# Performance work log

Hardware: AMD Instinct MI355X
Metric: run time of the kernel (lower is better)

The kernel has to match this reference:

```python
import jax, jax.numpy as jnp
import numpy as np

N = 50000      # nodes
E = 800000     # edges
GENE = 64      # gene_dim
HID = 128      # hidden_dim
NCLS = 10      # num_classes
EPS = 1e-5


def setup_inputs() -> dict:
    key = jax.random.key(0)
    ks = jax.random.split(key, 4)
    inp = {
        "x": jax.random.normal(ks[0], (N, GENE), jnp.float32),
        "edge_index": jax.random.randint(ks[1], (2, E), 0, N),
    }
    # PNA-style conv: concat([x, 4 aggregators x 3 scalers]) -> 13*d_in features
    dims = [(GENE, HID), (HID, 2 * HID), (2 * HID, HID), (HID, HID // 2)]
    for i, (din, dout) in enumerate(dims, 1):
        k = jax.random.fold_in(key, i)
        inp[f"W{i}"] = jax.random.normal(k, (13 * din, dout), jnp.float32) / float(np.sqrt(13 * din))
        inp[f"b{i}"] = jnp.zeros((dout,), jnp.float32)
        inp[f"gamma{i}"] = jnp.ones((dout,), jnp.float32)
        inp[f"beta{i}"] = jnp.zeros((dout,), jnp.float32)
    inp["Wc"] = jax.random.normal(ks[2], (HID // 2, NCLS), jnp.float32) / float(np.sqrt(HID // 2))
    inp["bc"] = jnp.zeros((NCLS,), jnp.float32)
    return inp


def _pna(x, src, dst, deg, log_deg, delta, W, b):
    # gather source features along edges: [E, d]
    msg = x[src]
    cnt = jnp.maximum(deg, 1.0)[:, None]
    s = jax.ops.segment_sum(msg, dst, num_segments=N)
    mean = s / cnt
    mean_sq = jax.ops.segment_sum(msg * msg, dst, num_segments=N) / cnt
    std = jnp.sqrt(jnp.maximum(mean_sq - mean * mean, 0.0) + EPS)
    has = (deg > 0)[:, None]
    mn = jnp.where(has, jax.ops.segment_min(msg, dst, num_segments=N), 0.0)
    mx = jnp.where(has, jax.ops.segment_max(msg, dst, num_segments=N), 0.0)
    aggs = jnp.concatenate([mean, mn, mx, std], axis=-1)  # [N, 4d]
    amp = (log_deg / delta)[:, None]                       # amplification scaler
    att = jnp.where(log_deg > 0, delta / jnp.maximum(log_deg, 1e-6), 1.0)[:, None]
    feat = jnp.concatenate([x, aggs, aggs * amp, aggs * att], axis=-1)  # [N, 13d]
    return feat @ W + b


def _bn(h, gamma, beta):
    m = h.mean(axis=0)
    v = h.var(axis=0)
    return (h - m) / jnp.sqrt(v + EPS) * gamma + beta


def reference(x, edge_index, W1, b1, gamma1, beta1, W2, b2, gamma2, beta2,
              W3, b3, gamma3, beta3, W4, b4, gamma4, beta4, Wc, bc):
    src, dst = edge_index[0], edge_index[1]
    deg = jax.ops.segment_sum(jnp.ones((E,), jnp.float32), dst, num_segments=N)
    log_deg = jnp.log1p(deg)
    delta = log_deg.mean()
    h = _pna(x, src, dst, deg, log_deg, delta, W1, b1)
    h = _bn(jax.nn.relu(h), gamma1, beta1)
    h = _pna(h, src, dst, deg, log_deg, delta, W2, b2)
    h = _bn(jax.nn.relu(h), gamma2, beta2)
    h = _pna(h, src, dst, deg, log_deg, delta, W3, b3)
    h = _bn(jax.nn.relu(h), gamma3, beta3)
    h = _pna(h, src, dst, deg, log_deg, delta, W4, b4)
    h = _bn(jax.nn.relu(h), gamma4, beta4)
    return h @ Wc + bc
```

## Files before the change

kernel.cpp:

```cpp
#include <hip/hip_runtime.h>
#include <hip/hip_bf16.h>

#define NN 50000
#define NE 800000
#define EPSV 1e-5f
#define NB 49

typedef _Float16 h8 __attribute__((ext_vector_type(8)));
typedef float    f4 __attribute__((ext_vector_type(4)));


__global__ void k_deg(const int* __restrict__ dst, int* __restrict__ deg){
  int e = blockIdx.x*blockDim.x + threadIdx.x;
  if(e < NE) atomicAdd(&deg[dst[e]], 1);
}

__global__ void k_logdeg(const int* __restrict__ deg, float* __restrict__ logdeg,
                         float* __restrict__ dsum){
  int i = blockIdx.x*blockDim.x + threadIdx.x;
  float v = 0.f;
  if(i < NN){ v = log1pf((float)deg[i]); logdeg[i] = v; }
  __shared__ float sh[256];
  sh[threadIdx.x] = v; __syncthreads();
  for(int off=128; off>0; off>>=1){
    if(threadIdx.x < off) sh[threadIdx.x] += sh[threadIdx.x+off];
    __syncthreads();
  }
  if(threadIdx.x == 0) atomicAdd(dsum, sh[0]);
}

__global__ void k_scalers(const float* __restrict__ logdeg, const float* __restrict__ dsum,
                          float* __restrict__ amp, float* __restrict__ att){
  int i = blockIdx.x*blockDim.x + threadIdx.x;
  if(i >= NN) return;
  float delta = dsum[0] / (float)NN;
  float ld = logdeg[i];
  amp[i] = ld / delta;
  att[i] = (ld > 0.f) ? (delta / fmaxf(ld, 1e-6f)) : 1.f;
}

__global__ void k_scan1(const int* __restrict__ deg, int* __restrict__ rowptr,
                        int* __restrict__ bsum){
  __shared__ int buf[1024];
  int tid = threadIdx.x;
  int i = blockIdx.x*1024 + tid;
  int v = (i < NN) ? deg[i] : 0;
  buf[tid] = v; __syncthreads();
  for(int off=1; off<1024; off<<=1){
    int t = (tid >= off) ? buf[tid-off] : 0;
    __syncthreads();
    buf[tid] += t;
    __syncthreads();
  }
  if(i < NN) rowptr[i] = buf[tid] - v;
  if(tid == 1023) bsum[blockIdx.x] = buf[1023];
}

__global__ void k_scan2(int* __restrict__ bsum){
  if(threadIdx.x == 0){
    int s = 0;
    for(int b = 0; b < NB; b++){ int t = bsum[b]; bsum[b] = s; s += t; }
    bsum[NB] = s;
  }
}

__global__ void k_scan3(int* __restrict__ rowptr, int* __restrict__ cursor,
                        const int* __restrict__ bsum){
  int i = blockIdx.x*256 + threadIdx.x;
  if(i < NN){
    int v = rowptr[i] + bsum[i >> 10];
    rowptr[i] = v; cursor[i] = v;
  }
  if(i == NN) rowptr[NN] = bsum[NB];
}

__global__ void k_fill(const int* __restrict__ src, const int* __restrict__ dst,
                       int* __restrict__ cursor, int* __restrict__ colidx){
  int e = blockIdx.x*blockDim.x + threadIdx.x;
  if(e < NE){
    int pos = atomicAdd(&cursor[dst[e]], 1);
    colidx[pos] = src[e];
  }
}

__global__ void k_cvtx(const float* __restrict__ x, _Float16* __restrict__ act){
  int i = blockIdx.x*256 + threadIdx.x;
  if(i < NN*64) act[i] = (_Float16)x[i];
}

__global__ void k_coef_id(float* __restrict__ cs, float* __restrict__ csh,
                          _Float16* __restrict__ cs16, _Float16* __restrict__ csh16){
  int c = threadIdx.x;
  cs[c] = 1.f; csh[c] = 0.f;
  cs16[c] = (_Float16)1.f; csh16[c] = (_Float16)0.f;
}

__global__ void k_bn_coef(const float* __restrict__ colsum, const float* __restrict__ colss,
                          const float* __restrict__ gamma, const float* __restrict__ beta,
                          int dout, float* __restrict__ cs, float* __restrict__ csh,
                          _Float16* __restrict__ cs16, _Float16* __restrict__ csh16){
  int c = threadIdx.x;
  if(c >= dout) return;
  float mean = colsum[c] / (float)NN;
  float var  = colss[c] / (float)NN - mean*mean;
  float inv  = rsqrtf(fmaxf(var, 0.f) + EPSV);
  float a = inv * gamma[c];
  float b = beta[c] - mean * a;
  cs[c] = a; csh[c] = b;
  cs16[c] = (_Float16)a; csh16[c] = (_Float16)b;
}


template<int D>
__global__ __launch_bounds__(256) void k_agg8(
    const _Float16* __restrict__ act,
    const int* __restrict__ rowptr, const int* __restrict__ colidx,
    const float* __restrict__ cs, const float* __restrict__ csh,
    _Float16* __restrict__ aggs, size_t aggN)
{
  constexpr int LPN = D >> 3;
  constexpr int NPW = 64 / LPN;
  int wv = threadIdx.x >> 6, lane = threadIdx.x & 63;
  int n = blockIdx.x*(NPW*4) + wv*NPW + (lane / LPN);
  int c = (lane % LPN) * 8;
  if(n >= NN) return;
  int beg = rowptr[n], end = rowptr[n+1];
  const _Float16* hp = act + c;

  float s[8], q[8], mn[8], mx[8];
  #pragma unroll
  for(int j = 0; j < 8; j++){ s[j]=0.f; q[j]=0.f; mn[j]=INFINITY; mx[j]=-INFINITY; }

#define ACC8(v) { _Pragma("unroll") for(int j=0;j<8;j++){ float a=(float)(v)[j]; \
    s[j]+=a; q[j]+=a*a; mn[j]=fminf(mn[j],a); mx[j]=fmaxf(mx[j],a); } }

  int e = beg;
  for(; e+8 <= end; e+=8){
    int i0=colidx[e],   i1=colidx[e+1], i2=colidx[e+2], i3=colidx[e+3];
    int i4=colidx[e+4], i5=colidx[e+5], i6=colidx[e+6], i7=colidx[e+7];
    h8 v0 = *(const h8*)(hp + (size_t)i0*D);
    h8 v1 = *(const h8*)(hp + (size_t)i1*D);
    h8 v2 = *(const h8*)(hp + (size_t)i2*D);
    h8 v3 = *(const h8*)(hp + (size_t)i3*D);
    h8 v4 = *(const h8*)(hp + (size_t)i4*D);
    h8 v5 = *(const h8*)(hp + (size_t)i5*D);
    h8 v6 = *(const h8*)(hp + (size_t)i6*D);
    h8 v7 = *(const h8*)(hp + (size_t)i7*D);
    ACC8(v0) ACC8(v1) ACC8(v2) ACC8(v3) ACC8(v4) ACC8(v5) ACC8(v6) ACC8(v7)
  }
  for(; e+4 <= end; e+=4){
    int i0=colidx[e], i1=colidx[e+1], i2=colidx[e+2], i3=colidx[e+3];
    h8 v0 = *(const h8*)(hp + (size_t)i0*D);
    h8 v1 = *(const h8*)(hp + (size_t)i1*D);
    h8 v2 = *(const h8*)(hp + (size_t)i2*D);
    h8 v3 = *(const h8*)(hp + (size_t)i3*D);
    ACC8(v0) ACC8(v1) ACC8(v2) ACC8(v3)
  }
  for(; e < end; e++){
    h8 v = *(const h8*)(hp + (size_t)colidx[e]*D);
    ACC8(v)
  }
#undef ACC8

  float cnt = (end>beg) ? (float)(end-beg) : 1.f;
  h8 vm, vn, vx, vs;
  #pragma unroll
  for(int j = 0; j < 8; j++){
    float a = cs[c+j], b = csh[c+j];
    float mean_r = s[j]/cnt;
    float var_r  = fmaxf(q[j]/cnt - mean_r*mean_r, 0.f);
    float meanp = a*mean_r + b;
    float mnp = (a >= 0.f) ? a*mn[j]+b : a*mx[j]+b;
    float mxp = (a >= 0.f) ? a*mx[j]+b : a*mn[j]+b;
    float sdp = sqrtf(a*a*var_r + EPSV);
    if(end <= beg){ meanp = 0.f; mnp = 0.f; mxp = 0.f; sdp = sqrtf(EPSV); }
    vm[j] = (_Float16)meanp; vn[j] = (_Float16)mnp;
    vx[j] = (_Float16)mxp;   vs[j] = (_Float16)sdp;
  }

  _Float16* dst = aggs + (size_t)(c>>6)*aggN + (size_t)n*256 + (c & 63);
  *(h8*)(dst)       = vm;
  *(h8*)(dst + 64)  = vn;
  *(h8*)(dst + 128) = vx;
  *(h8*)(dst + 192) = vs;
}


struct PackJob { const float* W; _Float16* dst; int d, o, j0, start; };
struct PackArgs { PackJob job[9]; int total; };

__global__ void k_pack_all(PackArgs a){
  int idx = blockIdx.x*256 + threadIdx.x;
  if(idx >= a.total) return;
  int ji = 0;
  while(ji < 8 && idx >= a.job[ji+1].start) ji++;
  PackJob J = a.job[ji];
  int rel = idx - J.start;
  int j    = rel & 7;
  int lane = (rel >> 3) & 63;
  int rem  = rel >> 9;
  int ntiles = J.o >> 4;
  int kb = rem / ntiles;
  int nt = rem - kb*ntiles;
  int k = kb*32 + (lane>>4)*8 + j;
  int n = nt*16 + (lane&15);
  int srcrow;
  if(k < 64)       srcrow = J.j0 + k;
  else if(k < 320){ int t=k-64;  srcrow = (1+(t>>6))*J.d + J.j0 + (t&63); }
  else if(k < 576){ int t=k-320; srcrow = (5+(t>>6))*J.d + J.j0 + (t&63); }
  else            { int t=k-576; srcrow = (9+(t>>6))*J.d + J.j0 + (t&63); }
  J.dst[rel] = (_Float16)J.W[(size_t)srcrow*J.o + n];
}


template<int NCH>
__global__ __launch_bounds__(256) void k_mfma_fused(
    const _Float16* __restrict__ actIn,
    const _Float16* __restrict__ aggs,
    const float* __restrict__ amp, const float* __restrict__ att,
    const _Float16* __restrict__ cs16, const _Float16* __restrict__ csh16,
    const _Float16* __restrict__ Wp, int o,
    const float* __restrict__ bias,
    _Float16* __restrict__ out,
    float* __restrict__ colsum, float* __restrict__ colss)
{
  constexpr int D = NCH * 64;
  __shared__ float redS[64], redQ[64];
  int tid  = threadIdx.x;
  int wv   = tid >> 6;
  int lane = tid & 63;
  int mi   = lane & 15;
  int q    = lane >> 4;
  int m0   = blockIdx.y * 128 + wv * 32;
  int c0   = blockIdx.x * 64;
  int ntiles = o >> 4;
  int nt0  = blockIdx.x * 4;

  if(tid < 64){ redS[tid] = 0.f; redQ[tid] = 0.f; }

  int mrow[2];
  mrow[0] = min(m0 + mi,      NN-1);
  mrow[1] = min(m0 + 16 + mi, NN-1);
  _Float16 am16[2] = { (_Float16)amp[mrow[0]], (_Float16)amp[mrow[1]] };
  _Float16 at16[2] = { (_Float16)att[mrow[0]], (_Float16)att[mrow[1]] };
  const _Float16* hAb[2];
  const _Float16* agb[2];
  hAb[0] = actIn + (size_t)mrow[0]*D + q*8;
  hAb[1] = actIn + (size_t)mrow[1]*D + q*8;
  agb[0] = aggs + (size_t)mrow[0]*256 + q*8;
  agb[1] = aggs + (size_t)mrow[1]*256 + q*8;

  f4 acc[2][4] = {};
  const size_t aggN = (size_t)NN*256;

  #pragma unroll
  for(int c = 0; c < NCH; c++){
    const _Float16* Wpc = Wp + (size_t)c*832*o;
    auto bfrag = [&](int kb, int nn) -> h8 {
      return *(const h8*)(Wpc + (((size_t)kb*ntiles + nt0 + nn)*64 + lane)*8);
    };

    h8 ax[2][2];
    h8 ag[8][2];
    #pragma unroll
    for(int kb = 0; kb < 2; kb++){
      h8 sc = *(const h8*)(cs16  + c*64 + kb*32 + q*8);
      h8 sh = *(const h8*)(csh16 + c*64 + kb*32 + q*8);
      #pragma unroll
      for(int t = 0; t < 2; t++){
        h8 a = *(const h8*)(hAb[t] + c*64 + kb*32);
        ax[kb][t] = a*sc + sh;
      }
    }
    #pragma unroll
    for(int idx = 0; idx < 8; idx++)
      #pragma unroll
      for(int t = 0; t < 2; t++)
        ag[idx][t] = *(const h8*)(agb[t] + (size_t)c*aggN + idx*32);

    #pragma unroll
    for(int kb = 0; kb < 2; kb++)
      #pragma unroll
      for(int t = 0; t < 2; t++)
        #pragma unroll
        for(int nn = 0; nn < 4; nn++)
          acc[t][nn] = __builtin_amdgcn_mfma_f32_16x16x32_f16(ax[kb][t], bfrag(kb,nn), acc[t][nn], 0,0,0);

    #pragma unroll
    for(int idx = 0; idx < 8; idx++){
      #pragma unroll
      for(int t = 0; t < 2; t++){
        h8 apl = ag[idx][t];
        h8 aam = apl * am16[t];
        h8 aat = apl * at16[t];
        #pragma unroll
        for(int nn = 0; nn < 4; nn++){
          acc[t][nn] = __builtin_amdgcn_mfma_f32_16x16x32_f16(apl, bfrag(2+idx,  nn), acc[t][nn], 0,0,0);
          acc[t][nn] = __builtin_amdgcn_mfma_f32_16x16x32_f16(aam, bfrag(10+idx, nn), acc[t][nn], 0,0,0);
          acc[t][nn] = __builtin_amdgcn_mfma_f32_16x16x32_f16(aat, bfrag(18+idx, nn), acc[t][nn], 0,0,0);
        }
      }
    }
  }

  __syncthreads();

  #pragma unroll
  for(int nn = 0; nn < 4; nn++){
    int n = c0 + nn*16 + mi;
    float bv = bias[n];
    float ps = 0.f, pq = 0.f;
    #pragma unroll
    for(int t = 0; t < 2; t++){
      #pragma unroll
      for(int r = 0; r < 4; r++){
        int m = m0 + t*16 + q*4 + r;
        if(m < NN){
          float v = fmaxf(bv + acc[t][nn][r], 0.f);
          out[(size_t)m*o + n] = (_Float16)v;
          ps += v; pq += v*v;
        }
      }
    }
    ps += __shfl_xor(ps, 16); pq += __shfl_xor(pq, 16);
    ps += __shfl_xor(ps, 32); pq += __shfl_xor(pq, 32);
    if(q == 0){
      atomicAdd(&redS[nn*16 + mi], ps);
      atomicAdd(&redQ[nn*16 + mi], pq);
    }
  }
  __syncthreads();
  if(tid < 64){
    atomicAdd(&colsum[c0 + tid], redS[tid]);
    atomicAdd(&colss[c0 + tid],  redQ[tid]);
  }
}


__global__ __launch_bounds__(256) void k_cls(const _Float16* __restrict__ h,
    const float* __restrict__ cs, const float* __restrict__ csh,
    const float* __restrict__ Wc, const float* __restrict__ bc,
    float* __restrict__ out){
  __shared__ float w[640];
  __shared__ float bb[16];
  __shared__ float sca[64], shb[64];
  int tid = threadIdx.x;
  for(int i = tid; i < 640; i += 256) w[i] = Wc[i];
  if(tid < 10) bb[tid] = bc[tid];
  if(tid < 64){ sca[tid] = cs[tid]; shb[tid] = csh[tid]; }
  __syncthreads();
  int idx = blockIdx.x*256 + tid;
  int n = idx >> 4;
  int c = idx & 15;
  if(n < NN && c < 10){
    float acc = bb[c];
    const _Float16* hp = h + (size_t)n*64;
    #pragma unroll
    for(int k = 0; k < 64; k++)
      acc += ((float)hp[k]*sca[k] + shb[k]) * w[k*10 + c];
    out[(size_t)n*10 + c] = acc;
  }
}


extern "C" void kernel_launch(void* const* d_in, const int* in_sizes, int n_in,
                              void* d_out, int out_size, void* d_ws, size_t ws_size,
                              hipStream_t stream){
  const float* x = (const float*)d_in[0];
  const int* edge = (const int*)d_in[1];
  const int* esrc = edge;
  const int* edst = edge + NE;
  const float* W[4]  = {(const float*)d_in[2],  (const float*)d_in[6],
                        (const float*)d_in[10], (const float*)d_in[14]};
  const float* bb[4] = {(const float*)d_in[3],  (const float*)d_in[7],
                        (const float*)d_in[11], (const float*)d_in[15]};
  const float* gm[4] = {(const float*)d_in[4],  (const float*)d_in[8],
                        (const float*)d_in[12], (const float*)d_in[16]};
  const float* bt[4] = {(const float*)d_in[5],  (const float*)d_in[9],
                        (const float*)d_in[13], (const float*)d_in[17]};
  const float* Wc = (const float*)d_in[18];
  const float* bc = (const float*)d_in[19];
  (void)in_sizes; (void)n_in; (void)out_size; (void)ws_size;

  char* p = (char*)d_ws;
  auto alloc = [&](size_t bytes)->char*{
    char* r = p; p += (bytes + 255) & ~(size_t)255; return r;
  };
  _Float16* act0 = (_Float16*)alloc((size_t)NN*256*2);
  _Float16* act1 = (_Float16*)alloc((size_t)NN*256*2);
  _Float16* aggs = (_Float16*)alloc((size_t)4*NN*256*2);
  int*   deg    = (int*)  alloc((size_t)NN*4);
  float* logdeg = (float*)alloc((size_t)NN*4);
  float* amp    = (float*)alloc((size_t)NN*4);
  float* att    = (float*)alloc((size_t)NN*4);
  int*   rowptr = (int*)  alloc((size_t)(NN+1)*4);
  int*   cursor = (int*)  alloc((size_t)NN*4);
  int*   colidx = (int*)  alloc((size_t)NE*4);
  int*   bsum   = (int*)  alloc((size_t)(NB+1)*4);
  float* colsumL= (float*)alloc(4*256*4);
  float* colssL = (float*)alloc(4*256*4);
  float* dsum   = (float*)alloc(256);
  float*    csA  = (float*)   alloc(256*4);
  float*    cshA = (float*)   alloc(256*4);
  float*    csB  = (float*)   alloc(256*4);
  float*    cshB = (float*)   alloc(256*4);
  _Float16* cs16A  = (_Float16*)alloc(256*2);
  _Float16* csh16A = (_Float16*)alloc(256*2);
  _Float16* cs16B  = (_Float16*)alloc(256*2);
  _Float16* csh16B = (_Float16*)alloc(256*2);

  const int din[4]  = {64, 128, 256, 128};
  const int dto[4]  = {128, 256, 128, 64};
  const size_t aggN = (size_t)NN*256;
  _Float16* WpL[4];
  PackArgs pa; int pj = 0, poff = 0;
  for(int l = 0; l < 4; l++){
    int nch = din[l]/64;
    WpL[l] = (_Float16*)alloc((size_t)nch*832*dto[l]*2);
    for(int c = 0; c < nch; c++){
      pa.job[pj] = { W[l], WpL[l] + (size_t)c*832*dto[l], din[l], dto[l], c*64, poff };
      poff += 832*dto[l]; pj++;
    }
  }
  pa.total = poff;

  hipMemsetAsync(deg, 0, (size_t)NN*4, stream);
  hipMemsetAsync(dsum, 0, 4, stream);
  hipMemsetAsync(colsumL, 0, 4*256*4, stream);
  hipMemsetAsync(colssL,  0, 4*256*4, stream);

  k_pack_all<<<(pa.total+255)/256, 256, 0, stream>>>(pa);
  k_deg     <<<(NE+255)/256, 256, 0, stream>>>(edst, deg);
  k_logdeg  <<<(NN+255)/256, 256, 0, stream>>>(deg, logdeg, dsum);
  k_scalers <<<(NN+255)/256, 256, 0, stream>>>(logdeg, dsum, amp, att);
  k_scan1   <<<NB, 1024, 0, stream>>>(deg, rowptr, bsum);
  k_scan2   <<<1, 64, 0, stream>>>(bsum);
  k_scan3   <<<(NN+256)/256, 256, 0, stream>>>(rowptr, cursor, bsum);
  k_fill    <<<(NE+255)/256, 256, 0, stream>>>(esrc, edst, cursor, colidx);
  k_cvtx    <<<(NN*64+255)/256, 256, 0, stream>>>(x, act0);
  k_coef_id <<<1, 256, 0, stream>>>(csA, cshA, cs16A, csh16A);

  _Float16* actIn = act0;  _Float16* actOut = act1;
  float *csI = csA, *cshI = cshA, *csO = csB, *cshO = cshB;
  _Float16 *cs16I = cs16A, *csh16I = csh16A, *cs16O = cs16B, *csh16O = csh16B;

  for(int l = 0; l < 4; l++){
    int d = din[l], o = dto[l];
    int npb = (64 / (d >> 3)) * 4;
    int nagg = (NN + npb - 1) / npb;
    dim3 g(o/64, (NN+127)/128);
    float* csum = colsumL + l*256;
    float* csq  = colssL + l*256;
    switch(d){
      case 64:
        k_agg8<64><<<nagg, 256, 0, stream>>>(actIn, rowptr, colidx, csI, cshI, aggs, aggN);
        k_mfma_fused<1><<<g, 256, 0, stream>>>(actIn, aggs, amp, att, cs16I, csh16I,
                                               WpL[l], o, bb[l], actOut, csum, csq);
        break;
      case 128:
        k_agg8<128><<<nagg, 256, 0, stream>>>(actIn, rowptr, colidx, csI, cshI, aggs, aggN);
        k_mfma_fused<2><<<g, 256, 0, stream>>>(actIn, aggs, amp, att, cs16I, csh16I,
                                               WpL[l], o, bb[l], actOut, csum, csq);
        break;
      default:
        k_agg8<256><<<nagg, 256, 0, stream>>>(actIn, rowptr, colidx, csI, cshI, aggs, aggN);
        k_mfma_fused<4><<<g, 256, 0, stream>>>(actIn, aggs, amp, att, cs16I, csh16I,
                                               WpL[l], o, bb[l], actOut, csum, csq);
        break;
    }
    k_bn_coef<<<1, 256, 0, stream>>>(csum, csq, gm[l], bt[l], o,
                                     csO, cshO, cs16O, csh16O);
    _Float16* ta = actIn; actIn = actOut; actOut = ta;
    float* tf;
    tf = csI;  csI = csO;  csO = tf;
    tf = cshI; cshI = cshO; cshO = tf;
    _Float16* th;
    th = cs16I;  cs16I = cs16O;  cs16O = th;
    th = csh16I; csh16I = csh16O; csh16O = th;
  }
  k_cls<<<(NN*16+255)/256, 256, 0, stream>>>(actIn, csI, cshI, Wc, bc, (float*)d_out);
}
```

Baseline: 698.4 us.

## Double-buffer MFMA weight fragments in LDS via async global_load_lds

The fused PNA matmul kernel now stages weight B-fragments into a double-buffered shared-memory tile using asynchronous global-to-LDS loads, one phase ahead. The A operands (activations and aggregates) are also prefetched into registers for the next phase. The K loop is restructured into 9 phases per 64-wide chunk, with a block barrier after each phase. The aim is to overlap weight and activation loads with MFMA work and share weights across the four waves. The cost is many more barriers, extra LDS traffic, and lower register-level prefetch depth than the old approach of loading all aggregates at once.

Result: faster. 656.0 us (-6.1%).

```diff
diff --git a/kernel.cpp b/kernel.cpp
--- a/kernel.cpp
+++ b/kernel.cpp
@@ -8,6 +8,13 @@
 
 typedef _Float16 h8 __attribute__((ext_vector_type(8)));
 typedef float    f4 __attribute__((ext_vector_type(4)));
+
+#define AS1 __attribute__((address_space(1)))
+#define AS3 __attribute__((address_space(3)))
+
+__device__ __forceinline__ void gload_lds16(const _Float16* g, _Float16* l){
+  __builtin_amdgcn_global_load_lds((const AS1 void*)g, (AS3 void*)l, 16, 0, 0);
+}
 
 
 __global__ void k_deg(const int* __restrict__ dst, int* __restrict__ deg){
@@ -222,9 +229,12 @@
     const _Float16* __restrict__ Wp, int o,
     const float* __restrict__ bias,
     _Float16* __restrict__ out,
-    float* __restrict__ colsum, float* __restrict__ colss)
+    float* __restrict__ colsum, float* __restrict__ colss,
+    size_t aggN)
 {
   constexpr int D = NCH * 64;
+  constexpr int NPH = NCH * 9;
+  __shared__ _Float16 Bsm[2][12*512];
   __shared__ float redS[64], redQ[64];
   int tid  = threadIdx.x;
   int wv   = tid >> 6;
@@ -251,59 +261,102 @@
   agb[1] = aggs + (size_t)mrow[1]*256 + q*8;
 
   f4 acc[2][4] = {};
-  const size_t aggN = (size_t)NN*256;
+
+  auto stageX = [&](_Float16* buf, int c){
+    const _Float16* Wpc = Wp + (size_t)c*832*o;
+    #pragma unroll
+    for(int s = 0; s < 2; s++){
+      int ti = wv*2 + s;
+      int kb = ti >> 2, nn = ti & 3;
+      gload_lds16(Wpc + (((size_t)kb*ntiles + nt0 + nn)*64 + lane)*8,
+                  buf + ti*512);
+    }
+  };
+  auto stageP = [&](_Float16* buf, int c, int idx){
+    const _Float16* Wpc = Wp + (size_t)c*832*o;
+    #pragma unroll
+    for(int s = 0; s < 3; s++){
+      int ti = wv*3 + s;
+      int kj = ti >> 2, nn = ti & 3;
+      int kb = (kj == 0 ? 2 : (kj == 1 ? 10 : 18)) + idx;
+      gload_lds16(Wpc + (((size_t)kb*ntiles + nt0 + nn)*64 + lane)*8,
+                  buf + ti*512);
+    }
+  };
+
+  h8 pA[4]; h8 pS[2]; h8 pH[2];
+  auto loadA = [&](int c, int sub){
+    if(sub == 0){
+      #pragma unroll
+      for(int kb = 0; kb < 2; kb++){
+        pS[kb] = *(const h8*)(cs16  + c*64 + kb*32 + q*8);
+        pH[kb] = *(const h8*)(csh16 + c*64 + kb*32 + q*8);
+        #pragma unroll
+        for(int t = 0; t < 2; t++)
+          pA[kb*2+t] = *(const h8*)(hAb[t] + c*64 + kb*32);
+      }
+    } else {
+      int idx = sub - 1;
+      #pragma unroll
+      for(int t = 0; t < 2; t++)
+        pA[t] = *(const h8*)(agb[t] + (size_t)c*aggN + idx*32);
+    }
+  };
+
+  stageX(&Bsm[0][0], 0);
+  loadA(0, 0);
+  __syncthreads();
 
   #pragma unroll
-  for(int c = 0; c < NCH; c++){
-    const _Float16* Wpc = Wp + (size_t)c*832*o;
-    auto bfrag = [&](int kb, int nn) -> h8 {
-      return *(const h8*)(Wpc + (((size_t)kb*ntiles + nt0 + nn)*64 + lane)*8);
-    };
-
-    h8 ax[2][2];
-    h8 ag[8][2];
-    #pragma unroll
-    for(int kb = 0; kb < 2; kb++){
-      h8 sc = *(const h8*)(cs16  + c*64 + kb*32 + q*8);
-      h8 sh = *(const h8*)(csh16 + c*64 + kb*32 + q*8);
+  for(int ph = 0; ph < NPH; ph++){
+    const int c   = ph / 9;
+    const int sub = ph % 9;
+    _Float16* cur = &Bsm[ph & 1][0];
+    _Float16* nxt = &Bsm[(ph & 1) ^ 1][0];
+
+    h8 cA[4] = { pA[0], pA[1], pA[2], pA[3] };
+    h8 cS[2] = { pS[0], pS[1] };
+    h8 cH[2] = { pH[0], pH[1] };
+
+    if(ph + 1 < NPH){
+      const int c2   = (ph + 1) / 9;
+      const int sub2 = (ph + 1) % 9;
+      if(sub2 == 0) stageX(nxt, c2);
+      else          stageP(nxt, c2, sub2 - 1);
+      loadA(c2, sub2);
+    }
+
+    if(sub == 0){
+      #pragma unroll
+      for(int kb = 0; kb < 2; kb++)
+        #pragma unroll
+        for(int t = 0; t < 2; t++){
+          h8 ax = cA[kb*2+t]*cS[kb] + cH[kb];
+          #pragma unroll
+          for(int nn = 0; nn < 4; nn++)
+            acc[t][nn] = __builtin_amdgcn_mfma_f32_16x16x32_f16(
+                ax, *(const h8*)(cur + (kb*4+nn)*512 + lane*8), acc[t][nn], 0,0,0);
+        }
+    } else {
       #pragma unroll
       for(int t = 0; t < 2; t++){
-        h8 a = *(const h8*)(hAb[t] + c*64 + kb*32);
-        ax[kb][t] = a*sc + sh;
-      }
-    }
-    #pragma unroll
-    for(int idx = 0; idx < 8; idx++)
-      #pragma unroll
-      for(int t = 0; t < 2; t++)
-        ag[idx][t] = *(const h8*)(agb[t] + (size_t)c*aggN + idx*32);
-
-    #pragma unroll
-    for(int kb = 0; kb < 2; kb++)
-      #pragma unroll
-      for(int t = 0; t < 2; t++)
-        #pragma unroll
-        for(int nn = 0; nn < 4; nn++)
-          acc[t][nn] = __builtin_amdgcn_mfma_f32_16x16x32_f16(ax[kb][t], bfrag(kb,nn), acc[t][nn], 0,0,0);
-
-    #pragma unroll
-    for(int idx = 0; idx < 8; idx++){
-      #pragma unroll
-      for(int t = 0; t < 2; t++){
-        h8 apl = ag[idx][t];
+        h8 apl = cA[t];
         h8 aam = apl * am16[t];
         h8 aat = apl * at16[t];
         #pragma unroll
         for(int nn = 0; nn < 4; nn++){
-          acc[t][nn] = __builtin_amdgcn_mfma_f32_16x16x32_f16(apl, bfrag(2+idx,  nn), acc[t][nn], 0,0,0);
-          acc[t][nn] = __builtin_amdgcn_mfma_f32_16x16x32_f16(aam, bfrag(10+idx, nn), acc[t][nn], 0,0,0);
-          acc[t][nn] = __builtin_amdgcn_mfma_f32_16x16x32_f16(aat, bfrag(18+idx, nn), acc[t][nn], 0,0,0);
+          acc[t][nn] = __builtin_amdgcn_mfma_f32_16x16x32_f16(
+              apl, *(const h8*)(cur + (0*4+nn)*512 + lane*8), acc[t][nn], 0,0,0);
+          acc[t][nn] = __builtin_amdgcn_mfma_f32_16x16x32_f16(
+              aam, *(const h8*)(cur + (4+nn)*512 + lane*8), acc[t][nn], 0,0,0);
+          acc[t][nn] = __builtin_amdgcn_mfma_f32_16x16x32_f16(
+              aat, *(const h8*)(cur + (8+nn)*512 + lane*8), acc[t][nn], 0,0,0);
         }
       }
     }
-  }
-
-  __syncthreads();
+
+    __syncthreads();
+  }
 
   #pragma unroll
   for(int nn = 0; nn < 4; nn++){
@@ -455,17 +508,17 @@
       case 64:
         k_agg8<64><<<nagg, 256, 0, stream>>>(actIn, rowptr, colidx, csI, cshI, aggs, aggN);
         k_mfma_fused<1><<<g, 256, 0, stream>>>(actIn, aggs, amp, att, cs16I, csh16I,
-                                               WpL[l], o, bb[l], actOut, csum, csq);
+                                               WpL[l], o, bb[l], actOut, csum, csq, aggN);
         break;
       case 128:
         k_agg8<128><<<nagg, 256, 0, stream>>>(actIn, rowptr, colidx, csI, cshI, aggs, aggN);
         k_mfma_fused<2><<<g, 256, 0, stream>>>(actIn, aggs, amp, att, cs16I, csh16I,
-                                               WpL[l], o, bb[l], actOut, csum, csq);
+                                               WpL[l], o, bb[l], actOut, csum, csq, aggN);
         break;
       default:
         k_agg8<256><<<nagg, 256, 0, stream>>>(actIn, rowptr, colidx, csI, cshI, aggs, aggN);
         k_mfma_fused<4><<<g, 256, 0, stream>>>(actIn, aggs, amp, att, cs16I, csh16I,
-                                               WpL[l], o, bb[l], actOut, csum, csq);
+                                               WpL[l], o, bb[l], actOut, csum, csq, aggN);
         break;
     }
     k_bn_coef<<<1, 256, 0, stream>>>(csum, csq, gm[l], bt[l], o,
```
